# Performance work log

Measured on AMD Instinct MI355X. Metric: run time of the kernel, lower is better.

## Reference

```python
import jax, jax.numpy as jnp
import numpy as np

D_MODEL = 512
NUM_HEADS = 8
WINDOW = 64
HEAD_DIM = D_MODEL // NUM_HEADS


def setup_inputs() -> dict:
    key = jax.random.key(0)
    k1, k2, k3 = jax.random.split(key, 3)
    B, F, L, D = 4, 16, 2048, D_MODEL
    x = jax.random.normal(k1, (B, F, L, D), dtype=jnp.float32)
    w_qkv = jax.random.normal(k2, (D, 3 * D), dtype=jnp.float32) * (1.0 / np.sqrt(D))
    b_qkv = jnp.zeros((3 * D,), dtype=jnp.float32)
    w_proj = jax.random.normal(k3, (D, D), dtype=jnp.float32) * (1.0 / np.sqrt(D))
    b_proj = jnp.zeros((D,), dtype=jnp.float32)
    return {"x": x, "w_qkv": w_qkv, "b_qkv": b_qkv, "w_proj": w_proj, "b_proj": b_proj}


def reference(x, w_qkv, b_qkv, w_proj, b_proj):
    B, F, L, D = x.shape
    W = WINDOW
    H, hd = NUM_HEADS, HEAD_DIM
    nw = L // W  # L chosen divisible by window_size; pad path is identity here
    # partition into windows: (B, F, nw, W, D)
    xw = x.reshape(B, F, nw, W, D)
    # fused QKV projection
    qkv = jnp.einsum('bfnwd,de->bfnwe', xw, w_qkv) + b_qkv  # (B,F,nw,W,3D)
    qkv = qkv.reshape(B, F, nw, W, 3, H, hd)
    q = qkv[..., 0, :, :]  # (B,F,nw,W,H,hd)
    k = qkv[..., 1, :, :]
    v = qkv[..., 2, :, :]
    scale = 1.0 / np.sqrt(hd).astype(np.float32)
    # per-window attention: scores (B,F,nw,H,W,W)
    scores = jnp.einsum('bfnqhd,bfnkhd->bfnhqk', q, k) * scale
    attn = jax.nn.softmax(scores, axis=-1)
    out = jnp.einsum('bfnhqk,bfnkhd->bfnqhd', attn, v)  # (B,F,nw,W,H,hd)
    out = out.reshape(B, F, nw, W, D)
    out = jnp.einsum('bfnwd,de->bfnwe', out, w_proj) + b_proj
    return out.reshape(B, F, L, D)
```

## Files before the change

kernel.cpp:

```cpp
#include <hip/hip_runtime.h>

typedef __attribute__((ext_vector_type(8))) short short8;
typedef __attribute__((ext_vector_type(4))) float f32x4;
typedef unsigned short u16;
typedef unsigned int u32;

__device__ __forceinline__ u16 f2bf(float f){
  union { float f; u32 u; } v; v.f = f;
  u32 u = v.u;
  u32 r = (u + 0x7FFFu + ((u >> 16) & 1u)) >> 16;
  return (u16)r;
}

__device__ __forceinline__ u32 cvtpk(float a, float b){
  u32 r;
  asm("v_cvt_pk_bf16_f32 %0, %1, %2" : "=v"(r) : "v"(a), "v"(b));
  return r;
}

__device__ __forceinline__ int swz(int row, int cb){ return cb ^ ((row & 7) << 4); }

__device__ __forceinline__ void gload16(const void* g, void* l){
  __builtin_amdgcn_global_load_lds(
      (const __attribute__((address_space(1))) unsigned int*)g,
      (__attribute__((address_space(3))) unsigned int*)l, 16, 0, 0);
}

__global__ void convert_weights_frag(const float* __restrict__ wqkv,
                                     const float* __restrict__ wproj,
                                     u16* __restrict__ wqf,
                                     u16* __restrict__ wpf){
  int c = blockIdx.x * 256 + threadIdx.x;
  union { u16 u[8]; uint4 v; } t;
  if (c < 98304){
    int bn = c >> 13;
    int r  = c & 8191;
    int kt = r >> 10;
    int q  = r & 1023;
    int nsub = q >> 7;
    int ks = (q >> 6) & 1;
    int l  = q & 63;
    int e  = bn*128 + nsub*16 + (l & 15);
    int k0 = kt*64 + ks*32 + (l >> 4)*8;
    #pragma unroll
    for (int i = 0; i < 8; ++i) t.u[i] = f2bf(wqkv[(long)(k0 + i) * 1536 + e]);
    *reinterpret_cast<uint4*>(wqf + (long)c * 8) = t.v;
  } else {
    int c2 = c - 98304;
    int cb = c2 >> 12;
    int r  = c2 & 4095;
    int hh = r >> 9;
    int q  = r & 511;
    int n  = q >> 7;
    int ks = (q >> 6) & 1;
    int l  = q & 63;
    int e  = cb*64 + n*16 + (l & 15);
    int k0 = hh*64 + ks*32 + (l >> 4)*8;
    #pragma unroll
    for (int i = 0; i < 8; ++i) t.u[i] = f2bf(wproj[(long)(k0 + i) * 512 + e]);
    *reinterpret_cast<uint4*>(wpf + (long)c2 * 8) = t.v;
  }
}

__global__ void convert_x(const float* __restrict__ x, u16* __restrict__ xbf){
  int c = blockIdx.x * 256 + threadIdx.x;
  int tile = c >> 10, row = (c >> 3) & 127, c7 = c & 7;
  int bm = tile >> 3, kt = tile & 7;
  int j  = c7 ^ (row & 7);
  const float* src = x + (long)(bm * 128 + row) * 512 + kt * 64 + j * 8;
  float4 v0 = *reinterpret_cast<const float4*>(src);
  float4 v1 = *reinterpret_cast<const float4*>(src + 4);
  union { u16 u[8]; uint4 v; } t;
  t.u[0] = f2bf(v0.x); t.u[1] = f2bf(v0.y); t.u[2] = f2bf(v0.z); t.u[3] = f2bf(v0.w);
  t.u[4] = f2bf(v1.x); t.u[5] = f2bf(v1.y); t.u[6] = f2bf(v1.z); t.u[7] = f2bf(v1.w);
  *reinterpret_cast<uint4*>(xbf + (long)c * 8) = t.v;
}

__global__ __launch_bounds__(256, 3) void qkv_gemm128(
    const u16*  __restrict__ xbf,
    const u16*  __restrict__ wqf,
    const float* __restrict__ bqkv,
    u16* __restrict__ qkv)
{
  __shared__ char smem[34816];

  const int tid = threadIdx.x;
  const int l = tid & 63, w = tid >> 6;
  const int g = l >> 4,  ln = l & 15;
  const int wm = w >> 1, wn = w & 1;

  int hb   = blockIdx.x;
  int work = (hb & 7) * 1536 + (hb >> 3);
  int bn   = work % 12;
  int bm   = work / 12;

  f32x4 acc[4][4];
  #pragma unroll
  for (int m = 0; m < 4; ++m)
    #pragma unroll
    for (int n = 0; n < 4; ++n) acc[m][n] = (f32x4){0.f,0.f,0.f,0.f};

  const char* abase = (const char*)(xbf + (long)(bm * 8) * 8192);
  const u16*  bbase = wqf + (long)bn * 65536;

  auto stageA = [&](int kt, int slot){
    const char* src = abase + (long)kt * 16384;
    char* dst = smem + slot * 16384;
    #pragma unroll
    for (int i = 0; i < 4; ++i)
      gload16(src + (i*256 + tid)*16, dst + i*4096 + w*1024);
  };

  stageA(0, 0); stageA(1, 1);
  asm volatile("s_waitcnt vmcnt(4)" ::: "memory");
  __builtin_amdgcn_s_barrier();

  for (int t = 0; t < 8; ++t){
    short8 b[4][2];
    #pragma unroll
    for (int n = 0; n < 4; ++n)
      #pragma unroll
      for (int ks = 0; ks < 2; ++ks)
        b[n][ks] = *reinterpret_cast<const short8*>(
            bbase + ((((long)t*8 + wn*4 + n)*2 + ks)*64 + l)*8);
    const char* Ab = smem + (t & 1) * 16384;
    short8 a[4][2];
    #pragma unroll
    for (int m = 0; m < 4; ++m){
      int r = wm*64 + m*16 + ln;
      #pragma unroll
      for (int ks = 0; ks < 2; ++ks)
        a[m][ks] = *reinterpret_cast<const short8*>(
            Ab + r*128 + (((ks*4 + g) ^ (r & 7)) << 4));
    }
    asm volatile("s_waitcnt lgkmcnt(0)" ::: "memory");
    __builtin_amdgcn_s_barrier();
    if (t < 6) stageA(t + 2, t & 1);
    __builtin_amdgcn_s_setprio(1);
    #pragma unroll
    for (int m = 0; m < 4; ++m)
      #pragma unroll
      for (int n = 0; n < 4; ++n)
        #pragma unroll
        for (int ks = 0; ks < 2; ++ks)
          acc[m][n] = __builtin_amdgcn_mfma_f32_16x16x32_bf16(
              a[m][ks], b[n][ks], acc[m][n], 0, 0, 0);
    __builtin_amdgcn_s_setprio(0);
    if (t < 6)       asm volatile("s_waitcnt vmcnt(4)" ::: "memory");
    else if (t == 6) asm volatile("s_waitcnt vmcnt(0)" ::: "memory");
    if (t < 7) __builtin_amdgcn_s_barrier();
  }

  u16* ldsC = (u16*)smem;
  #pragma unroll
  for (int n = 0; n < 4; ++n){
    int col  = wn*64 + n*16 + ln;
    float bias = bqkv[bn*128 + col];
    #pragma unroll
    for (int m = 0; m < 4; ++m){
      int r0 = wm*64 + m*16 + g*4;
      #pragma unroll
      for (int r = 0; r < 4; ++r)
        ldsC[(r0 + r) * 136 + col] = f2bf(acc[m][n][r] + bias);
    }
  }
  __syncthreads();
  {
    int row = tid >> 1, half = tid & 1;
    const char* src = (const char*)(ldsC + row * 136 + half * 64);
    char* dst = (char*)qkv + ((long)(bm*128 + row) * 1536 + bn*128 + half*64) * 2;
    #pragma unroll
    for (int j = 0; j < 8; ++j)
      *reinterpret_cast<uint4*>(dst + j*16) = *reinterpret_cast<const uint4*>(src + j*16);
  }
}

__global__ __launch_bounds__(512, 4) void winattn_proj(
    const u16* __restrict__ qkv,
    const u16* __restrict__ wpf,
    const float* __restrict__ bproj,
    float* __restrict__ out)
{
  __shared__ u16 lds[8][4096];
  const int tid = threadIdx.x;
  const int l = tid & 63, w = tid >> 6;
  const int g = l >> 4,  ln = l & 15;
  const int gh = g >> 1, gl = g & 1;
  const long tokb = (long)blockIdx.x * 64;
  u16* vt = lds[w];
  const int h = w;

  {
    const int dg = l & 3, tg = l >> 2;
    uint4 vr[4][2];
    #pragma unroll
    for (int r = 0; r < 4; ++r){
      const char* vrow = (const char*)(qkv + (tokb + tg*4 + r) * 1536 + 1024 + h*64 + dg*16);
      vr[r][0] = *reinterpret_cast<const uint4*>(vrow);
      vr[r][1] = *reinterpret_cast<const uint4*>(vrow + 16);
    }
    #pragma unroll
    for (int dd = 0; dd < 16; ++dd){
      int d = dg*16 + dd;
      int sub = dd & 7, hi = dd >> 3;
      uint2 pk;
      pk.x = (u32)((const u16*)&vr[0][hi])[sub] | ((u32)((const u16*)&vr[1][hi])[sub] << 16);
      pk.y = (u32)((const u16*)&vr[2][hi])[sub] | ((u32)((const u16*)&vr[3][hi])[sub] << 16);
      *reinterpret_cast<uint2*>((char*)vt + d*128 + swz(d, tg*8)) = pk;
    }
  }

  f32x4 oacc[4][4];
  #pragma unroll
  for (int m = 0; m < 4; ++m)
    #pragma unroll
    for (int n = 0; n < 4; ++n) oacc[m][n] = (f32x4){0.f,0.f,0.f,0.f};

  const int lnA = ln + 32*gl;

  #pragma unroll
  for (int half = 0; half < 2; ++half){
    short8 qa[2][2];
    #pragma unroll
    for (int j = 0; j < 2; ++j){
      const char* qrow = (const char*)(qkv + (tokb + (half*2+j)*16 + ln) * 1536 + h*64 + g*8);
      qa[j][0] = *reinterpret_cast<const short8*>(qrow);
      qa[j][1] = *reinterpret_cast<const short8*>(qrow + 64);
    }
    f32x4 st[4][2];
    #pragma unroll
    for (int mk = 0; mk < 4; ++mk){
      st[mk][0] = (f32x4){0.f,0.f,0.f,0.f};
      st[mk][1] = (f32x4){0.f,0.f,0.f,0.f};
    }
    #pragma unroll
    for (int mk = 0; mk < 4; ++mk){
      const char* krow = (const char*)(qkv + (tokb + mk*16 + ln) * 1536 + 512 + h*64 + g*8);
      short8 kb0 = *reinterpret_cast<const short8*>(krow);
      short8 kb1 = *reinterpret_cast<const short8*>(krow + 64);
      #pragma unroll
      for (int j = 0; j < 2; ++j){
        st[mk][j] = __builtin_amdgcn_mfma_f32_16x16x32_bf16(kb0, qa[j][0], st[mk][j], 0, 0, 0);
        st[mk][j] = __builtin_amdgcn_mfma_f32_16x16x32_bf16(kb1, qa[j][1], st[mk][j], 0, 0, 0);
      }
    }
    u32 warr[4][2][2];
    #pragma unroll
    for (int j = 0; j < 2; ++j){
      float mx = -3.4e38f;
      #pragma unroll
      for (int mk = 0; mk < 4; ++mk)
        #pragma unroll
        for (int r = 0; r < 4; ++r) mx = fmaxf(mx, st[mk][j][r]);
      mx = fmaxf(mx, __shfl_xor(mx, 16, 64));
      mx = fmaxf(mx, __shfl_xor(mx, 32, 64));
      float s = 0.f;
      #pragma unroll
      for (int mk = 0; mk < 4; ++mk)
        #pragma unroll
        for (int r = 0; r < 4; ++r){
          float p = __expf((st[mk][j][r] - mx) * 0.125f);
          st[mk][j][r] = p; s += p;
        }
      s += __shfl_xor(s, 16, 64);
      s += __shfl_xor(s, 32, 64);
      float inv = 1.f / s;
      #pragma unroll
      for (int mk = 0; mk < 4; ++mk){
        warr[mk][j][0] = cvtpk(st[mk][j][0]*inv, st[mk][j][1]*inv);
        warr[mk][j][1] = cvtpk(st[mk][j][2]*inv, st[mk][j][3]*inv);
      }
    }
    __builtin_amdgcn_s_setprio(1);
    #pragma unroll
    for (int ks = 0; ks < 2; ++ks){
      short8 vb[4];
      #pragma unroll
      for (int n = 0; n < 4; ++n){
        int row = n*16 + ln;
        vb[n] = *reinterpret_cast<const short8*>((char*)vt + row*128 + swz(row, (ks*32 + g*8)*2));
      }
      #pragma unroll
      for (int mo = 0; mo < 2; ++mo){
        int m = half*2 + mo;
        u32 c0a = warr[2*ks  ][mo][0], c0b = warr[2*ks  ][mo][1];
        u32 c1a = warr[2*ks+1][mo][0], c1b = warr[2*ks+1][mo][1];
        u32 s0a = (u32)__shfl((int)c0a, lnA, 64);
        u32 s1a = (u32)__shfl((int)c1a, lnA, 64);
        u32 s0b = (u32)__shfl((int)c0b, lnA, 64);
        u32 s1b = (u32)__shfl((int)c1b, lnA, 64);
        u32 t0a = (u32)__shfl((int)c0a, lnA+16, 64);
        u32 t1a = (u32)__shfl((int)c1a, lnA+16, 64);
        u32 t0b = (u32)__shfl((int)c0b, lnA+16, 64);
        u32 t1b = (u32)__shfl((int)c1b, lnA+16, 64);
        union { u32 u[4]; short8 v; } pf;
        pf.u[0] = gh ? s1a : s0a;
        pf.u[1] = gh ? s1b : s0b;
        pf.u[2] = gh ? t1a : t0a;
        pf.u[3] = gh ? t1b : t0b;
        #pragma unroll
        for (int n = 0; n < 4; ++n)
          oacc[m][n] = __builtin_amdgcn_mfma_f32_16x16x32_bf16(pf.v, vb[n], oacc[m][n], 0, 0, 0);
      }
    }
    __builtin_amdgcn_s_setprio(0);
  }

  #pragma unroll
  for (int m = 0; m < 4; ++m)
    #pragma unroll
    for (int n = 0; n < 4; ++n){
      int d = n*16 + ln;
      #pragma unroll
      for (int r = 0; r < 4; ++r){
        int t = m*16 + g*4 + r;
        *reinterpret_cast<u16*>((char*)vt + t*128 + swz(t, d*2)) = f2bf(oacc[m][n][r]);
      }
    }

  __syncthreads();

  f32x4 acc[4][4];
  #pragma unroll
  for (int m = 0; m < 4; ++m)
    #pragma unroll
    for (int n = 0; n < 4; ++n) acc[m][n] = (f32x4){0.f,0.f,0.f,0.f};

  for (int hh = 0; hh < 8; ++hh){
    const char* obuf = (const char*)lds[hh];
    #pragma unroll
    for (int ks = 0; ks < 2; ++ks){
      short8 a[4], b[4];
      #pragma unroll
      for (int m = 0; m < 4; ++m){
        int row = m*16 + ln;
        a[m] = *reinterpret_cast<const short8*>(obuf + row*128 + swz(row, (ks*32 + g*8)*2));
      }
      #pragma unroll
      for (int n = 0; n < 4; ++n)
        b[n] = *reinterpret_cast<const short8*>(
            wpf + ((((long)w*8 + hh)*4 + n)*2 + ks)*512 + (long)l*8);
      __builtin_amdgcn_s_setprio(1);
      #pragma unroll
      for (int m = 0; m < 4; ++m)
        #pragma unroll
        for (int n = 0; n < 4; ++n)
          acc[m][n] = __builtin_amdgcn_mfma_f32_16x16x32_bf16(a[m], b[n], acc[m][n], 0, 0, 0);
      __builtin_amdgcn_s_setprio(0);
    }
  }

  #pragma unroll
  for (int n = 0; n < 4; ++n){
    int col = w*64 + n*16 + ln;
    float bias = bproj[col];
    #pragma unroll
    for (int m = 0; m < 4; ++m){
      #pragma unroll
      for (int r = 0; r < 4; ++r){
        int t = m*16 + g*4 + r;
        out[(tokb + t) * 512 + col] = acc[m][n][r] + bias;
      }
    }
  }
}

__global__ void convert_weights(const float* __restrict__ wqkv,
                                const float* __restrict__ wproj,
                                u16* __restrict__ wqkvt,
                                u16* __restrict__ wprojt){
  int tid = blockIdx.x * 256 + threadIdx.x;
  union { u16 u[8]; uint4 v; } tmp;
  if (tid < 1536 * 64){
    int e  = tid >> 6;
    int kc = (tid & 63) << 3;
    #pragma unroll
    for (int i = 0; i < 8; ++i) tmp.u[i] = f2bf(wqkv[(long)(kc + i) * 1536 + e]);
    *reinterpret_cast<uint4*>(wqkvt + (long)e * 512 + kc) = tmp.v;
  } else {
    int t2 = tid - 1536 * 64;
    int c  = t2 >> 6;
    int kc = (t2 & 63) << 3;
    #pragma unroll
    for (int i = 0; i < 8; ++i) tmp.u[i] = f2bf(wproj[(long)(kc + i) * 512 + c]);
    *reinterpret_cast<uint4*>(wprojt + (long)c * 512 + kc) = tmp.v;
  }
}

__global__ __launch_bounds__(512, 2) void fused_winattn(
    const float* __restrict__ x,
    const u16*  __restrict__ wqkvt,
    const float* __restrict__ bqkv,
    const u16*  __restrict__ wprojt,
    const float* __restrict__ bproj,
    float* __restrict__ out)
{
  __shared__ u16 lds_x[64 * 512];
  __shared__ u16 lds_q[64 * 64];
  __shared__ u16 lds_k[64 * 64];
  __shared__ u16 lds_vt[64 * 64];
  __shared__ u16 lds_p[64 * 64];

  const int tid = threadIdx.x;
  const int l   = tid & 63;
  const int w   = tid >> 6;
  const int g   = l >> 4;
  const int ln  = l & 15;
  const long tokbase = (long)blockIdx.x * 64;

  {
    const float4* xv = reinterpret_cast<const float4*>(x + tokbase * 512);
    #pragma unroll
    for (int j = 0; j < 16; ++j){
      int i   = j * 512 + tid;
      int row = i >> 7;
      int c4  = i & 127;
      float4 v = xv[i];
      uint2 pk;
      pk.x = (u32)f2bf(v.x) | ((u32)f2bf(v.y) << 16);
      pk.y = (u32)f2bf(v.z) | ((u32)f2bf(v.w) << 16);
      int byte = row * 1024 + swz(row, c4 * 8);
      *reinterpret_cast<uint2*>(reinterpret_cast<char*>(lds_x) + byte) = pk;
    }
  }

  f32x4 oacc[4][4];
  #pragma unroll
  for (int m = 0; m < 4; ++m)
    #pragma unroll
    for (int n = 0; n < 4; ++n) oacc[m][n] = (f32x4){0.f, 0.f, 0.f, 0.f};

  const int mw   = w & 3;
  const int half = w >> 2;

  __syncthreads();

  for (int h = 0; h < 8; ++h){
    f32x4 qacc[6];
    #pragma unroll
    for (int j = 0; j < 6; ++j) qacc[j] = (f32x4){0.f, 0.f, 0.f, 0.f};
    int ebase[6];
    #pragma unroll
    for (int j = 0; j < 6; ++j){
      int nt = half * 6 + j;
      int sec = nt >> 2;
      ebase[j] = sec * 512 + h * 64 + (nt & 3) * 16;
    }
    const int arow = mw * 16 + ln;
    #pragma unroll
    for (int ks = 0; ks < 16; ++ks){
      short8 a = *reinterpret_cast<const short8*>(
          reinterpret_cast<const char*>(lds_x) + arow * 1024 + swz(arow, (ks * 32 + g * 8) * 2));
      #pragma unroll
      for (int j = 0; j < 6; ++j){
        short8 b = *reinterpret_cast<const short8*>(
            wqkvt + (long)(ebase[j] + ln) * 512 + ks * 32 + g * 8);
        qacc[j] = __builtin_amdgcn_mfma_f32_16x16x32_bf16(a, b, qacc[j], 0, 0, 0);
      }
    }
    #pragma unroll
    for (int j = 0; j < 6; ++j){
      int nt  = half * 6 + j;
      int sec = nt >> 2;
      float bias = bqkv[ebase[j] + ln];
      if (sec < 2){
        u16* dst = (sec == 0) ? lds_q : lds_k;
        int c = (nt & 3) * 16 + ln;
        #pragma unroll
        for (int r = 0; r < 4; ++r){
          int t = mw * 16 + g * 4 + r;
          int byte = t * 128 + swz(t, c * 2);
          *reinterpret_cast<u16*>(reinterpret_cast<char*>(dst) + byte) = f2bf(qacc[j][r] + bias);
        }
      } else {
        int d  = (nt & 3) * 16 + ln;
        int t0 = mw * 16 + g * 4;
        uint2 pk;
        pk.x = (u32)f2bf(qacc[j][0] + bias) | ((u32)f2bf(qacc[j][1] + bias) << 16);
        pk.y = (u32)f2bf(qacc[j][2] + bias) | ((u32)f2bf(qacc[j][3] + bias) << 16);
        int byte = d * 128 + swz(d, t0 * 2);
        *reinterpret_cast<uint2*>(reinterpret_cast<char*>(lds_vt) + byte) = pk;
      }
    }
    __syncthreads();

    if (w < 4){
      f32x4 sacc[4];
      #pragma unroll
      for (int jt = 0; jt < 4; ++jt) sacc[jt] = (f32x4){0.f, 0.f, 0.f, 0.f};
      #pragma unroll
      for (int ks = 0; ks < 2; ++ks){
        int qrow = w * 16 + ln;
        short8 a = *reinterpret_cast<const short8*>(
            reinterpret_cast<const char*>(lds_q) + qrow * 128 + swz(qrow, (ks * 32 + g * 8) * 2));
        #pragma unroll
        for (int jt = 0; jt < 4; ++jt){
          int krow = jt * 16 + ln;
          short8 b = *reinterpret_cast<const short8*>(
              reinterpret_cast<const char*>(lds_k) + krow * 128 + swz(krow, (ks * 32 + g * 8) * 2));
          sacc[jt] = __builtin_amdgcn_mfma_f32_16x16x32_bf16(a, b, sacc[jt], 0, 0, 0);
        }
      }
      #pragma unroll
      for (int r = 0; r < 4; ++r){
        float mx = fmaxf(fmaxf(sacc[0][r], sacc[1][r]), fmaxf(sacc[2][r], sacc[3][r]));
        mx = fmaxf(mx, __shfl_xor(mx, 1, 64));
        mx = fmaxf(mx, __shfl_xor(mx, 2, 64));
        mx = fmaxf(mx, __shfl_xor(mx, 4, 64));
        mx = fmaxf(mx, __shfl_xor(mx, 8, 64));
        float p[4], s = 0.f;
        #pragma unroll
        for (int jt = 0; jt < 4; ++jt){
          p[jt] = __expf((sacc[jt][r] - mx) * 0.125f);
          s += p[jt];
        }
        s += __shfl_xor(s, 1, 64);
        s += __shfl_xor(s, 2, 64);
        s += __shfl_xor(s, 4, 64);
        s += __shfl_xor(s, 8, 64);
        float inv = 1.f / s;
        int i = w * 16 + g * 4 + r;
        #pragma unroll
        for (int jt = 0; jt < 4; ++jt){
          int c = jt * 16 + ln;
          int byte = i * 128 + swz(i, c * 2);
          *reinterpret_cast<u16*>(reinterpret_cast<char*>(lds_p) + byte) = f2bf(p[jt] * inv);
        }
      }
    }
    __syncthreads();

    {
      int mc  = w & 3;
      int nc0 = (w >> 2) * 2;
      f32x4 oc[2];
      oc[0] = (f32x4){0.f, 0.f, 0.f, 0.f};
      oc[1] = (f32x4){0.f, 0.f, 0.f, 0.f};
      #pragma unroll
      for (int ks = 0; ks < 2; ++ks){
        int prow = mc * 16 + ln;
        short8 a = *reinterpret_cast<const short8*>(
            reinterpret_cast<const char*>(lds_p) + prow * 128 + swz(prow, (ks * 32 + g * 8) * 2));
        #pragma unroll
        for (int jj = 0; jj < 2; ++jj){
          int vrow = (nc0 + jj) * 16 + ln;
          short8 b = *reinterpret_cast<const short8*>(
              reinterpret_cast<const char*>(lds_vt) + vrow * 128 + swz(vrow, (ks * 32 + g * 8) * 2));
          oc[jj] = __builtin_amdgcn_mfma_f32_16x16x32_bf16(a, b, oc[jj], 0, 0, 0);
        }
      }
      #pragma unroll
      for (int jj = 0; jj < 2; ++jj){
        int d = (nc0 + jj) * 16 + ln;
        #pragma unroll
        for (int r = 0; r < 4; ++r){
          int t = mc * 16 + g * 4 + r;
          int byte = t * 128 + swz(t, d * 2);
          *reinterpret_cast<u16*>(reinterpret_cast<char*>(lds_q) + byte) = f2bf(oc[jj][r]);
        }
      }
    }
    __syncthreads();

    #pragma unroll
    for (int ks = 0; ks < 2; ++ks){
      short8 a[4];
      #pragma unroll
      for (int m = 0; m < 4; ++m){
        int row = m * 16 + ln;
        a[m] = *reinterpret_cast<const short8*>(
            reinterpret_cast<const char*>(lds_q) + row * 128 + swz(row, (ks * 32 + g * 8) * 2));
      }
      #pragma unroll
      for (int nt = 0; nt < 4; ++nt){
        int e = w * 64 + nt * 16 + ln;
        short8 b = *reinterpret_cast<const short8*>(
            wprojt + (long)e * 512 + h * 64 + ks * 32 + g * 8);
        #pragma unroll
        for (int m = 0; m < 4; ++m)
          oacc[m][nt] = __builtin_amdgcn_mfma_f32_16x16x32_bf16(a[m], b, oacc[m][nt], 0, 0, 0);
      }
    }
    __syncthreads();
  }

  #pragma unroll
  for (int nt = 0; nt < 4; ++nt){
    int col = w * 64 + nt * 16 + ln;
    float bias = bproj[col];
    #pragma unroll
    for (int m = 0; m < 4; ++m){
      #pragma unroll
      for (int r = 0; r < 4; ++r){
        int t = m * 16 + g * 4 + r;
        out[(tokbase + t) * 512 + col] = oacc[m][nt][r] + bias;
      }
    }
  }
}

extern "C" void kernel_launch(void* const* d_in, const int* in_sizes, int n_in,
                              void* d_out, int out_size, void* d_ws, size_t ws_size,
                              hipStream_t stream) {
  const float* x     = (const float*)d_in[0];
  const float* wqkv  = (const float*)d_in[1];
  const float* bqkv  = (const float*)d_in[2];
  const float* wproj = (const float*)d_in[3];
  const float* bproj = (const float*)d_in[4];
  float* out = (float*)d_out;

  const size_t NEED = 538968064ULL;
  if (ws_size >= NEED){
    u16* wqf = (u16*)d_ws;
    u16* wpf = (u16*)((char*)d_ws + 1572864);
    u16* xbf = (u16*)((char*)d_ws + 2097152);
    u16* qkv = (u16*)((char*)d_ws + 136314880);
    convert_weights_frag<<<512, 256, 0, stream>>>(wqkv, wproj, wqf, wpf);
    convert_x<<<32768, 256, 0, stream>>>(x, xbf);
    qkv_gemm128<<<12288, 256, 0, stream>>>(xbf, wqf, bqkv, qkv);
    winattn_proj<<<2048, 512, 0, stream>>>(qkv, wpf, bproj, out);
  } else {
    u16* wqkvt  = (u16*)d_ws;
    u16* wprojt = wqkvt + 1536 * 512;
    convert_weights<<<512, 256, 0, stream>>>(wqkv, wproj, wqkvt, wprojt);
    fused_winattn<<<2048, 512, 0, stream>>>(x, wqkvt, bqkv, wprojt, bproj, out);
  }
}
```

Baseline: 582.6 us.

## Fuse x conversion, QKV GEMM, window attention and projection into one kernel

Replaces the separate x-to-bf16 conversion, QKV GEMM, and attention+projection kernels with a single kernel per 64-token window. The window's x rows are converted into LDS, and each wave (one head) computes its Q, K, V slices from weight fragments read directly from global memory, then runs attention and the output projection. This removes the large bf16 x and QKV intermediate round-trips through HBM and cuts the workspace requirement. In exchange it uses much more LDS per block (launch bounds drop to 2 blocks per CU) and loses the pipelined global-to-LDS staging of the old GEMM, so weight fragment loads may be less latency-hidden.

```diff
diff --git a/kernel.cpp b/kernel.cpp
--- a/kernel.cpp
+++ b/kernel.cpp
@@ -19,12 +19,6 @@
 }
 
 __device__ __forceinline__ int swz(int row, int cb){ return cb ^ ((row & 7) << 4); }
-
-__device__ __forceinline__ void gload16(const void* g, void* l){
-  __builtin_amdgcn_global_load_lds(
-      (const __attribute__((address_space(1))) unsigned int*)g,
-      (__attribute__((address_space(3))) unsigned int*)l, 16, 0, 0);
-}
 
 __global__ void convert_weights_frag(const float* __restrict__ wqkv,
                                      const float* __restrict__ wproj,
@@ -62,272 +56,236 @@
   }
 }
 
-__global__ void convert_x(const float* __restrict__ x, u16* __restrict__ xbf){
-  int c = blockIdx.x * 256 + threadIdx.x;
-  int tile = c >> 10, row = (c >> 3) & 127, c7 = c & 7;
-  int bm = tile >> 3, kt = tile & 7;
-  int j  = c7 ^ (row & 7);
-  const float* src = x + (long)(bm * 128 + row) * 512 + kt * 64 + j * 8;
-  float4 v0 = *reinterpret_cast<const float4*>(src);
-  float4 v1 = *reinterpret_cast<const float4*>(src + 4);
-  union { u16 u[8]; uint4 v; } t;
-  t.u[0] = f2bf(v0.x); t.u[1] = f2bf(v0.y); t.u[2] = f2bf(v0.z); t.u[3] = f2bf(v0.w);
-  t.u[4] = f2bf(v1.x); t.u[5] = f2bf(v1.y); t.u[6] = f2bf(v1.z); t.u[7] = f2bf(v1.w);
-  *reinterpret_cast<uint4*>(xbf + (long)c * 8) = t.v;
-}
-
-__global__ __launch_bounds__(256, 3) void qkv_gemm128(
-    const u16*  __restrict__ xbf,
+__global__ __launch_bounds__(512, 2) void fused_all(
+    const float* __restrict__ x,
     const u16*  __restrict__ wqf,
     const float* __restrict__ bqkv,
-    u16* __restrict__ qkv)
-{
-  __shared__ char smem[34816];
-
-  const int tid = threadIdx.x;
-  const int l = tid & 63, w = tid >> 6;
-  const int g = l >> 4,  ln = l & 15;
-  const int wm = w >> 1, wn = w & 1;
-
-  int hb   = blockIdx.x;
-  int work = (hb & 7) * 1536 + (hb >> 3);
-  int bn   = work % 12;
-  int bm   = work / 12;
-
-  f32x4 acc[4][4];
-  #pragma unroll
-  for (int m = 0; m < 4; ++m)
-    #pragma unroll
-    for (int n = 0; n < 4; ++n) acc[m][n] = (f32x4){0.f,0.f,0.f,0.f};
-
-  const char* abase = (const char*)(xbf + (long)(bm * 8) * 8192);
-  const u16*  bbase = wqf + (long)bn * 65536;
-
-  auto stageA = [&](int kt, int slot){
-    const char* src = abase + (long)kt * 16384;
-    char* dst = smem + slot * 16384;
-    #pragma unroll
-    for (int i = 0; i < 4; ++i)
-      gload16(src + (i*256 + tid)*16, dst + i*4096 + w*1024);
-  };
-
-  stageA(0, 0); stageA(1, 1);
-  asm volatile("s_waitcnt vmcnt(4)" ::: "memory");
-  __builtin_amdgcn_s_barrier();
-
-  for (int t = 0; t < 8; ++t){
-    short8 b[4][2];
-    #pragma unroll
-    for (int n = 0; n < 4; ++n)
-      #pragma unroll
-      for (int ks = 0; ks < 2; ++ks)
-        b[n][ks] = *reinterpret_cast<const short8*>(
-            bbase + ((((long)t*8 + wn*4 + n)*2 + ks)*64 + l)*8);
-    const char* Ab = smem + (t & 1) * 16384;
-    short8 a[4][2];
-    #pragma unroll
-    for (int m = 0; m < 4; ++m){
-      int r = wm*64 + m*16 + ln;
-      #pragma unroll
-      for (int ks = 0; ks < 2; ++ks)
-        a[m][ks] = *reinterpret_cast<const short8*>(
-            Ab + r*128 + (((ks*4 + g) ^ (r & 7)) << 4));
-    }
-    asm volatile("s_waitcnt lgkmcnt(0)" ::: "memory");
-    __builtin_amdgcn_s_barrier();
-    if (t < 6) stageA(t + 2, t & 1);
-    __builtin_amdgcn_s_setprio(1);
-    #pragma unroll
-    for (int m = 0; m < 4; ++m)
-      #pragma unroll
-      for (int n = 0; n < 4; ++n)
-        #pragma unroll
-        for (int ks = 0; ks < 2; ++ks)
-          acc[m][n] = __builtin_amdgcn_mfma_f32_16x16x32_bf16(
-              a[m][ks], b[n][ks], acc[m][n], 0, 0, 0);
-    __builtin_amdgcn_s_setprio(0);
-    if (t < 6)       asm volatile("s_waitcnt vmcnt(4)" ::: "memory");
-    else if (t == 6) asm volatile("s_waitcnt vmcnt(0)" ::: "memory");
-    if (t < 7) __builtin_amdgcn_s_barrier();
-  }
-
-  u16* ldsC = (u16*)smem;
-  #pragma unroll
-  for (int n = 0; n < 4; ++n){
-    int col  = wn*64 + n*16 + ln;
-    float bias = bqkv[bn*128 + col];
-    #pragma unroll
-    for (int m = 0; m < 4; ++m){
-      int r0 = wm*64 + m*16 + g*4;
-      #pragma unroll
-      for (int r = 0; r < 4; ++r)
-        ldsC[(r0 + r) * 136 + col] = f2bf(acc[m][n][r] + bias);
-    }
-  }
-  __syncthreads();
-  {
-    int row = tid >> 1, half = tid & 1;
-    const char* src = (const char*)(ldsC + row * 136 + half * 64);
-    char* dst = (char*)qkv + ((long)(bm*128 + row) * 1536 + bn*128 + half*64) * 2;
-    #pragma unroll
-    for (int j = 0; j < 8; ++j)
-      *reinterpret_cast<uint4*>(dst + j*16) = *reinterpret_cast<const uint4*>(src + j*16);
-  }
-}
-
-__global__ __launch_bounds__(512, 4) void winattn_proj(
-    const u16* __restrict__ qkv,
-    const u16* __restrict__ wpf,
+    const u16*  __restrict__ wpf,
     const float* __restrict__ bproj,
     float* __restrict__ out)
 {
-  __shared__ u16 lds[8][4096];
+  __shared__ u16 xw[64 * 512];
+  __shared__ u16 slots[8][4096];
+
   const int tid = threadIdx.x;
   const int l = tid & 63, w = tid >> 6;
   const int g = l >> 4,  ln = l & 15;
   const int gh = g >> 1, gl = g & 1;
   const long tokb = (long)blockIdx.x * 64;
-  u16* vt = lds[w];
   const int h = w;
+  u16* slot = slots[w];
 
   {
-    const int dg = l & 3, tg = l >> 2;
-    uint4 vr[4][2];
-    #pragma unroll
-    for (int r = 0; r < 4; ++r){
-      const char* vrow = (const char*)(qkv + (tokb + tg*4 + r) * 1536 + 1024 + h*64 + dg*16);
-      vr[r][0] = *reinterpret_cast<const uint4*>(vrow);
-      vr[r][1] = *reinterpret_cast<const uint4*>(vrow + 16);
-    }
-    #pragma unroll
-    for (int dd = 0; dd < 16; ++dd){
-      int d = dg*16 + dd;
-      int sub = dd & 7, hi = dd >> 3;
+    const float4* xv = reinterpret_cast<const float4*>(x + tokb * 512);
+    #pragma unroll
+    for (int i = 0; i < 16; ++i){
+      int idx = i * 512 + tid;
+      int row = idx >> 7, c4 = idx & 127;
+      float4 v = xv[idx];
       uint2 pk;
-      pk.x = (u32)((const u16*)&vr[0][hi])[sub] | ((u32)((const u16*)&vr[1][hi])[sub] << 16);
-      pk.y = (u32)((const u16*)&vr[2][hi])[sub] | ((u32)((const u16*)&vr[3][hi])[sub] << 16);
-      *reinterpret_cast<uint2*>((char*)vt + d*128 + swz(d, tg*8)) = pk;
-    }
-  }
-
-  f32x4 oacc[4][4];
-  #pragma unroll
-  for (int m = 0; m < 4; ++m)
-    #pragma unroll
-    for (int n = 0; n < 4; ++n) oacc[m][n] = (f32x4){0.f,0.f,0.f,0.f};
-
-  const int lnA = ln + 32*gl;
-
-  #pragma unroll
-  for (int half = 0; half < 2; ++half){
-    short8 qa[2][2];
-    #pragma unroll
-    for (int j = 0; j < 2; ++j){
-      const char* qrow = (const char*)(qkv + (tokb + (half*2+j)*16 + ln) * 1536 + h*64 + g*8);
-      qa[j][0] = *reinterpret_cast<const short8*>(qrow);
-      qa[j][1] = *reinterpret_cast<const short8*>(qrow + 64);
-    }
-    f32x4 st[4][2];
-    #pragma unroll
-    for (int mk = 0; mk < 4; ++mk){
-      st[mk][0] = (f32x4){0.f,0.f,0.f,0.f};
-      st[mk][1] = (f32x4){0.f,0.f,0.f,0.f};
-    }
-    #pragma unroll
-    for (int mk = 0; mk < 4; ++mk){
-      const char* krow = (const char*)(qkv + (tokb + mk*16 + ln) * 1536 + 512 + h*64 + g*8);
-      short8 kb0 = *reinterpret_cast<const short8*>(krow);
-      short8 kb1 = *reinterpret_cast<const short8*>(krow + 64);
-      #pragma unroll
-      for (int j = 0; j < 2; ++j){
-        st[mk][j] = __builtin_amdgcn_mfma_f32_16x16x32_bf16(kb0, qa[j][0], st[mk][j], 0, 0, 0);
-        st[mk][j] = __builtin_amdgcn_mfma_f32_16x16x32_bf16(kb1, qa[j][1], st[mk][j], 0, 0, 0);
-      }
-    }
-    u32 warr[4][2][2];
-    #pragma unroll
-    for (int j = 0; j < 2; ++j){
-      float mx = -3.4e38f;
-      #pragma unroll
-      for (int mk = 0; mk < 4; ++mk)
-        #pragma unroll
-        for (int r = 0; r < 4; ++r) mx = fmaxf(mx, st[mk][j][r]);
-      mx = fmaxf(mx, __shfl_xor(mx, 16, 64));
-      mx = fmaxf(mx, __shfl_xor(mx, 32, 64));
-      float s = 0.f;
-      #pragma unroll
-      for (int mk = 0; mk < 4; ++mk)
-        #pragma unroll
-        for (int r = 0; r < 4; ++r){
-          float p = __expf((st[mk][j][r] - mx) * 0.125f);
-          st[mk][j][r] = p; s += p;
-        }
-      s += __shfl_xor(s, 16, 64);
-      s += __shfl_xor(s, 32, 64);
-      float inv = 1.f / s;
-      #pragma unroll
-      for (int mk = 0; mk < 4; ++mk){
-        warr[mk][j][0] = cvtpk(st[mk][j][0]*inv, st[mk][j][1]*inv);
-        warr[mk][j][1] = cvtpk(st[mk][j][2]*inv, st[mk][j][3]*inv);
-      }
-    }
-    __builtin_amdgcn_s_setprio(1);
-    #pragma unroll
-    for (int ks = 0; ks < 2; ++ks){
-      short8 vb[4];
-      #pragma unroll
-      for (int n = 0; n < 4; ++n){
-        int row = n*16 + ln;
-        vb[n] = *reinterpret_cast<const short8*>((char*)vt + row*128 + swz(row, (ks*32 + g*8)*2));
-      }
-      #pragma unroll
-      for (int mo = 0; mo < 2; ++mo){
-        int m = half*2 + mo;
-        u32 c0a = warr[2*ks  ][mo][0], c0b = warr[2*ks  ][mo][1];
-        u32 c1a = warr[2*ks+1][mo][0], c1b = warr[2*ks+1][mo][1];
-        u32 s0a = (u32)__shfl((int)c0a, lnA, 64);
-        u32 s1a = (u32)__shfl((int)c1a, lnA, 64);
-        u32 s0b = (u32)__shfl((int)c0b, lnA, 64);
-        u32 s1b = (u32)__shfl((int)c1b, lnA, 64);
-        u32 t0a = (u32)__shfl((int)c0a, lnA+16, 64);
-        u32 t1a = (u32)__shfl((int)c1a, lnA+16, 64);
-        u32 t0b = (u32)__shfl((int)c0b, lnA+16, 64);
-        u32 t1b = (u32)__shfl((int)c1b, lnA+16, 64);
-        union { u32 u[4]; short8 v; } pf;
-        pf.u[0] = gh ? s1a : s0a;
-        pf.u[1] = gh ? s1b : s0b;
-        pf.u[2] = gh ? t1a : t0a;
-        pf.u[3] = gh ? t1b : t0b;
+      pk.x = cvtpk(v.x, v.y);
+      pk.y = cvtpk(v.z, v.w);
+      *reinterpret_cast<uint2*>(reinterpret_cast<char*>(xw) + row*1024 + swz(row, c4*8)) = pk;
+    }
+  }
+  __syncthreads();
+
+  f32x4 acc[4][4];
+  auto gemmQKV = [&](int s){
+    #pragma unroll
+    for (int m = 0; m < 4; ++m)
+      #pragma unroll
+      for (int n = 0; n < 4; ++n) acc[m][n] = (f32x4){0.f,0.f,0.f,0.f};
+    const u16* bb = wqf + (long)(s*4 + (h >> 1)) * 65536;
+    const int nsb = (h & 1) * 4;
+    #pragma unroll
+    for (int kk = 0; kk < 16; ++kk){
+      short8 bf[4], af[4];
+      #pragma unroll
+      for (int n = 0; n < 4; ++n)
+        bf[n] = *reinterpret_cast<const short8*>(
+            bb + ((((kk>>1)*8 + nsb + n)*2 + (kk & 1))*64 + l)*8);
+      #pragma unroll
+      for (int m = 0; m < 4; ++m){
+        int r = m*16 + ln;
+        af[m] = *reinterpret_cast<const short8*>(
+            reinterpret_cast<const char*>(xw) + r*1024 + swz(r, (kk*32 + g*8)*2));
+      }
+      __builtin_amdgcn_s_setprio(1);
+      #pragma unroll
+      for (int m = 0; m < 4; ++m)
         #pragma unroll
         for (int n = 0; n < 4; ++n)
-          oacc[m][n] = __builtin_amdgcn_mfma_f32_16x16x32_bf16(pf.v, vb[n], oacc[m][n], 0, 0, 0);
-      }
-    }
-    __builtin_amdgcn_s_setprio(0);
-  }
-
-  #pragma unroll
-  for (int m = 0; m < 4; ++m)
+          acc[m][n] = __builtin_amdgcn_mfma_f32_16x16x32_bf16(af[m], bf[n], acc[m][n], 0, 0, 0);
+      __builtin_amdgcn_s_setprio(0);
+    }
+  };
+
+  auto accToRows = [&](int boff){
     #pragma unroll
     for (int n = 0; n < 4; ++n){
       int d = n*16 + ln;
+      float bias = bqkv[boff + h*64 + d];
+      #pragma unroll
+      for (int m = 0; m < 4; ++m)
+        #pragma unroll
+        for (int r = 0; r < 4; ++r){
+          int t = m*16 + g*4 + r;
+          *reinterpret_cast<u16*>(reinterpret_cast<char*>(slot) + t*128 + swz(t, d*2)) =
+              f2bf(acc[m][n][r] + bias);
+        }
+    }
+  };
+
+  short8 qa[4][2], kb[4][2];
+
+  gemmQKV(0);
+  accToRows(0);
+  asm volatile("s_waitcnt lgkmcnt(0)" ::: "memory");
+  #pragma unroll
+  for (int j = 0; j < 4; ++j){
+    int r = j*16 + ln;
+    #pragma unroll
+    for (int ks = 0; ks < 2; ++ks)
+      qa[j][ks] = *reinterpret_cast<const short8*>(
+          reinterpret_cast<const char*>(slot) + r*128 + swz(r, (ks*32 + g*8)*2));
+  }
+  asm volatile("s_waitcnt lgkmcnt(0)" ::: "memory");
+
+  gemmQKV(1);
+  accToRows(512);
+  asm volatile("s_waitcnt lgkmcnt(0)" ::: "memory");
+  #pragma unroll
+  for (int mk = 0; mk < 4; ++mk){
+    int r = mk*16 + ln;
+    #pragma unroll
+    for (int ks = 0; ks < 2; ++ks)
+      kb[mk][ks] = *reinterpret_cast<const short8*>(
+          reinterpret_cast<const char*>(slot) + r*128 + swz(r, (ks*32 + g*8)*2));
+  }
+  asm volatile("s_waitcnt lgkmcnt(0)" ::: "memory");
+
+  gemmQKV(2);
+  #pragma unroll
+  for (int n = 0; n < 4; ++n){
+    int d = n*16 + ln;
+    float bias = bqkv[1024 + h*64 + d];
+    #pragma unroll
+    for (int m = 0; m < 4; ++m){
+      uint2 pk;
+      pk.x = cvtpk(acc[m][n][0] + bias, acc[m][n][1] + bias);
+      pk.y = cvtpk(acc[m][n][2] + bias, acc[m][n][3] + bias);
+      *reinterpret_cast<uint2*>(reinterpret_cast<char*>(slot) + d*128 + swz(d, (m*16 + g*4)*2)) = pk;
+    }
+  }
+  asm volatile("s_waitcnt lgkmcnt(0)" ::: "memory");
+
+  f32x4 st[4][4];
+  #pragma unroll
+  for (int mk = 0; mk < 4; ++mk)
+    #pragma unroll
+    for (int j = 0; j < 4; ++j) st[mk][j] = (f32x4){0.f,0.f,0.f,0.f};
+  __builtin_amdgcn_s_setprio(1);
+  #pragma unroll
+  for (int mk = 0; mk < 4; ++mk)
+    #pragma unroll
+    for (int j = 0; j < 4; ++j)
+      #pragma unroll
+      for (int ks = 0; ks < 2; ++ks)
+        st[mk][j] = __builtin_amdgcn_mfma_f32_16x16x32_bf16(kb[mk][ks], qa[j][ks], st[mk][j], 0, 0, 0);
+  __builtin_amdgcn_s_setprio(0);
+
+  u32 warr[4][4][2];
+  #pragma unroll
+  for (int j = 0; j < 4; ++j){
+    float mx = -3.4e38f;
+    #pragma unroll
+    for (int mk = 0; mk < 4; ++mk)
+      #pragma unroll
+      for (int r = 0; r < 4; ++r) mx = fmaxf(mx, st[mk][j][r]);
+    mx = fmaxf(mx, __shfl_xor(mx, 16, 64));
+    mx = fmaxf(mx, __shfl_xor(mx, 32, 64));
+    float s = 0.f;
+    #pragma unroll
+    for (int mk = 0; mk < 4; ++mk)
+      #pragma unroll
+      for (int r = 0; r < 4; ++r){
+        float p = __expf((st[mk][j][r] - mx) * 0.125f);
+        st[mk][j][r] = p; s += p;
+      }
+    s += __shfl_xor(s, 16, 64);
+    s += __shfl_xor(s, 32, 64);
+    float inv = 1.f / s;
+    #pragma unroll
+    for (int mk = 0; mk < 4; ++mk){
+      warr[mk][j][0] = cvtpk(st[mk][j][0]*inv, st[mk][j][1]*inv);
+      warr[mk][j][1] = cvtpk(st[mk][j][2]*inv, st[mk][j][3]*inv);
+    }
+  }
+
+  f32x4 oacc[4][4];
+  #pragma unroll
+  for (int m = 0; m < 4; ++m)
+    #pragma unroll
+    for (int n = 0; n < 4; ++n) oacc[m][n] = (f32x4){0.f,0.f,0.f,0.f};
+  const int lnA = ln + 32*gl;
+  #pragma unroll
+  for (int ks = 0; ks < 2; ++ks){
+    short8 vb[4];
+    #pragma unroll
+    for (int n = 0; n < 4; ++n){
+      int row = n*16 + ln;
+      vb[n] = *reinterpret_cast<const short8*>(
+          reinterpret_cast<const char*>(slot) + row*128 + swz(row, (ks*32 + g*8)*2));
+    }
+    __builtin_amdgcn_s_setprio(1);
+    #pragma unroll
+    for (int m = 0; m < 4; ++m){
+      u32 c0a = warr[2*ks  ][m][0], c0b = warr[2*ks  ][m][1];
+      u32 c1a = warr[2*ks+1][m][0], c1b = warr[2*ks+1][m][1];
+      u32 s0a = (u32)__shfl((int)c0a, lnA, 64);
+      u32 s1a = (u32)__shfl((int)c1a, lnA, 64);
+      u32 s0b = (u32)__shfl((int)c0b, lnA, 64);
+      u32 s1b = (u32)__shfl((int)c1b, lnA, 64);
+      u32 t0a = (u32)__shfl((int)c0a, lnA+16, 64);
+      u32 t1a = (u32)__shfl((int)c1a, lnA+16, 64);
+      u32 t0b = (u32)__shfl((int)c0b, lnA+16, 64);
+      u32 t1b = (u32)__shfl((int)c1b, lnA+16, 64);
+      union { u32 u[4]; short8 v; } pf;
+      pf.u[0] = gh ? s1a : s0a;
+      pf.u[1] = gh ? s1b : s0b;
+      pf.u[2] = gh ? t1a : t0a;
+      pf.u[3] = gh ? t1b : t0b;
+      #pragma unroll
+      for (int n = 0; n < 4; ++n)
+        oacc[m][n] = __builtin_amdgcn_mfma_f32_16x16x32_bf16(pf.v, vb[n], oacc[m][n], 0, 0, 0);
+    }
+    __builtin_amdgcn_s_setprio(0);
+  }
+
+  #pragma unroll
+  for (int m = 0; m < 4; ++m)
+    #pragma unroll
+    for (int n = 0; n < 4; ++n){
+      int d = n*16 + ln;
       #pragma unroll
       for (int r = 0; r < 4; ++r){
         int t = m*16 + g*4 + r;
-        *reinterpret_cast<u16*>((char*)vt + t*128 + swz(t, d*2)) = f2bf(oacc[m][n][r]);
+        *reinterpret_cast<u16*>(reinterpret_cast<char*>(slot) + t*128 + swz(t, d*2)) =
+            f2bf(oacc[m][n][r]);
       }
     }
 
   __syncthreads();
 
-  f32x4 acc[4][4];
+  f32x4 pacc[4][4];
   #pragma unroll
   for (int m = 0; m < 4; ++m)
     #pragma unroll
-    for (int n = 0; n < 4; ++n) acc[m][n] = (f32x4){0.f,0.f,0.f,0.f};
+    for (int n = 0; n < 4; ++n) pacc[m][n] = (f32x4){0.f,0.f,0.f,0.f};
 
   for (int hh = 0; hh < 8; ++hh){
-    const char* obuf = (const char*)lds[hh];
+    const char* obuf = (const char*)slots[hh];
     #pragma unroll
     for (int ks = 0; ks < 2; ++ks){
       short8 a[4], b[4];
@@ -345,7 +303,7 @@
       for (int m = 0; m < 4; ++m)
         #pragma unroll
         for (int n = 0; n < 4; ++n)
-          acc[m][n] = __builtin_amdgcn_mfma_f32_16x16x32_bf16(a[m], b[n], acc[m][n], 0, 0, 0);
+          pacc[m][n] = __builtin_amdgcn_mfma_f32_16x16x32_bf16(a[m], b[n], pacc[m][n], 0, 0, 0);
       __builtin_amdgcn_s_setprio(0);
     }
   }
@@ -359,7 +317,7 @@
       #pragma unroll
       for (int r = 0; r < 4; ++r){
         int t = m*16 + g*4 + r;
-        out[(tokb + t) * 512 + col] = acc[m][n][r] + bias;
+        out[(tokb + t) * 512 + col] = pacc[m][n][r] + bias;
       }
     }
   }
@@ -609,16 +567,12 @@
   const float* bproj = (const float*)d_in[4];
   float* out = (float*)d_out;
 
-  const size_t NEED = 538968064ULL;
+  const size_t NEED = 2097152ULL;
   if (ws_size >= NEED){
     u16* wqf = (u16*)d_ws;
     u16* wpf = (u16*)((char*)d_ws + 1572864);
-    u16* xbf = (u16*)((char*)d_ws + 2097152);
-    u16* qkv = (u16*)((char*)d_ws + 136314880);
     convert_weights_frag<<<512, 256, 0, stream>>>(wqkv, wproj, wqf, wpf);
-    convert_x<<<32768, 256, 0, stream>>>(x, xbf);
-    qkv_gemm128<<<12288, 256, 0, stream>>>(xbf, wqf, bqkv, qkv);
-    winattn_proj<<<2048, 512, 0, stream>>>(qkv, wpf, bproj, out);
+    fused_all<<<2048, 512, 0, stream>>>(x, wqf, bqkv, wpf, bproj, out);
   } else {
     u16* wqkvt  = (u16*)d_ws;
     u16* wprojt = wqkvt + 1536 * 512;
```

Result: slower. 643.1 us (+10.4%).

## Pre-fragment activations so QKV GEMM streams operands directly from global memory

Applied to the files above, without the earlier changes.

The bf16 conversion of x now writes activations in MFMA fragment order, mirroring the weight layout. The QKV GEMM then loads both A and B fragments directly from global memory into registers, dropping the LDS double-buffered staging, barriers and waitcnt choreography. LDS is now used only for the epilogue, and the occupancy hint rises to 4 blocks. The trade-off is that the two column-tile waves of a block each fetch the same A fragments from global/L2 with no shared LDS reuse, and there is no explicit prefetch overlap.

```diff
diff --git a/kernel.cpp b/kernel.cpp
--- a/kernel.cpp
+++ b/kernel.cpp
@@ -19,12 +19,6 @@
 }
 
 __device__ __forceinline__ int swz(int row, int cb){ return cb ^ ((row & 7) << 4); }
-
-__device__ __forceinline__ void gload16(const void* g, void* l){
-  __builtin_amdgcn_global_load_lds(
-      (const __attribute__((address_space(1))) unsigned int*)g,
-      (__attribute__((address_space(3))) unsigned int*)l, 16, 0, 0);
-}
 
 __global__ void convert_weights_frag(const float* __restrict__ wqkv,
                                      const float* __restrict__ wproj,
@@ -62,12 +56,16 @@
   }
 }
 
-__global__ void convert_x(const float* __restrict__ x, u16* __restrict__ xbf){
+__global__ void convert_x_frag(const float* __restrict__ x, u16* __restrict__ xbf){
   int c = blockIdx.x * 256 + threadIdx.x;
-  int tile = c >> 10, row = (c >> 3) & 127, c7 = c & 7;
-  int bm = tile >> 3, kt = tile & 7;
-  int j  = c7 ^ (row & 7);
-  const float* src = x + (long)(bm * 128 + row) * 512 + kt * 64 + j * 8;
+  int l    = c & 63;
+  int ks   = (c >> 6) & 1;
+  int msub = (c >> 7) & 7;
+  int kt   = (c >> 10) & 7;
+  int bm   = c >> 13;
+  int row  = bm*128 + msub*16 + (l & 15);
+  int k0   = kt*64 + ks*32 + (l >> 4)*8;
+  const float* src = x + (long)row * 512 + k0;
   float4 v0 = *reinterpret_cast<const float4*>(src);
   float4 v1 = *reinterpret_cast<const float4*>(src + 4);
   union { u16 u[8]; uint4 v; } t;
@@ -76,13 +74,13 @@
   *reinterpret_cast<uint4*>(xbf + (long)c * 8) = t.v;
 }
 
-__global__ __launch_bounds__(256, 3) void qkv_gemm128(
+__global__ __launch_bounds__(256, 4) void qkv_stream(
     const u16*  __restrict__ xbf,
     const u16*  __restrict__ wqf,
     const float* __restrict__ bqkv,
     u16* __restrict__ qkv)
 {
-  __shared__ char smem[34816];
+  __shared__ u16 ldsC[128 * 136];
 
   const int tid = threadIdx.x;
   const int l = tid & 63, w = tid >> 6;
@@ -100,42 +98,21 @@
     #pragma unroll
     for (int n = 0; n < 4; ++n) acc[m][n] = (f32x4){0.f,0.f,0.f,0.f};
 
-  const char* abase = (const char*)(xbf + (long)(bm * 8) * 8192);
-  const u16*  bbase = wqf + (long)bn * 65536;
-
-  auto stageA = [&](int kt, int slot){
-    const char* src = abase + (long)kt * 16384;
-    char* dst = smem + slot * 16384;
-    #pragma unroll
-    for (int i = 0; i < 4; ++i)
-      gload16(src + (i*256 + tid)*16, dst + i*4096 + w*1024);
-  };
-
-  stageA(0, 0); stageA(1, 1);
-  asm volatile("s_waitcnt vmcnt(4)" ::: "memory");
-  __builtin_amdgcn_s_barrier();
+  const u16* ap = xbf + (long)bm * 65536 + (((long)(wm*4)*2)*64 + l) * 8;
+  const u16* bp = wqf + (long)bn * 65536 + (((long)(wn*4)*2)*64 + l) * 8;
 
   for (int t = 0; t < 8; ++t){
-    short8 b[4][2];
+    short8 a[4][2], b[4][2];
+    #pragma unroll
+    for (int m = 0; m < 4; ++m)
+      #pragma unroll
+      for (int ks = 0; ks < 2; ++ks)
+        a[m][ks] = *reinterpret_cast<const short8*>(ap + ((m*2 + ks)*64)*8);
     #pragma unroll
     for (int n = 0; n < 4; ++n)
       #pragma unroll
       for (int ks = 0; ks < 2; ++ks)
-        b[n][ks] = *reinterpret_cast<const short8*>(
-            bbase + ((((long)t*8 + wn*4 + n)*2 + ks)*64 + l)*8);
-    const char* Ab = smem + (t & 1) * 16384;
-    short8 a[4][2];
-    #pragma unroll
-    for (int m = 0; m < 4; ++m){
-      int r = wm*64 + m*16 + ln;
-      #pragma unroll
-      for (int ks = 0; ks < 2; ++ks)
-        a[m][ks] = *reinterpret_cast<const short8*>(
-            Ab + r*128 + (((ks*4 + g) ^ (r & 7)) << 4));
-    }
-    asm volatile("s_waitcnt lgkmcnt(0)" ::: "memory");
-    __builtin_amdgcn_s_barrier();
-    if (t < 6) stageA(t + 2, t & 1);
+        b[n][ks] = *reinterpret_cast<const short8*>(bp + ((n*2 + ks)*64)*8);
     __builtin_amdgcn_s_setprio(1);
     #pragma unroll
     for (int m = 0; m < 4; ++m)
@@ -146,12 +123,10 @@
           acc[m][n] = __builtin_amdgcn_mfma_f32_16x16x32_bf16(
               a[m][ks], b[n][ks], acc[m][n], 0, 0, 0);
     __builtin_amdgcn_s_setprio(0);
-    if (t < 6)       asm volatile("s_waitcnt vmcnt(4)" ::: "memory");
-    else if (t == 6) asm volatile("s_waitcnt vmcnt(0)" ::: "memory");
-    if (t < 7) __builtin_amdgcn_s_barrier();
-  }
-
-  u16* ldsC = (u16*)smem;
+    ap += 8192;
+    bp += 8192;
+  }
+
   #pragma unroll
   for (int n = 0; n < 4; ++n){
     int col  = wn*64 + n*16 + ln;
@@ -616,8 +591,8 @@
     u16* xbf = (u16*)((char*)d_ws + 2097152);
     u16* qkv = (u16*)((char*)d_ws + 136314880);
     convert_weights_frag<<<512, 256, 0, stream>>>(wqkv, wproj, wqf, wpf);
-    convert_x<<<32768, 256, 0, stream>>>(x, xbf);
-    qkv_gemm128<<<12288, 256, 0, stream>>>(xbf, wqf, bqkv, qkv);
+    convert_x_frag<<<32768, 256, 0, stream>>>(x, xbf);
+    qkv_stream<<<12288, 256, 0, stream>>>(xbf, wqf, bqkv, qkv);
     winattn_proj<<<2048, 512, 0, stream>>>(qkv, wpf, bproj, out);
   } else {
     u16* wqkvt  = (u16*)d_ws;
```

Measured after the change: 807.7 us. +38.6%, slower.

## Fuse fp32-to-bf16 conversion of x into the QKV GEMM loader

Applied to the files above, without the earlier changes.

Removes the separate convert_x kernel and its bf16 workspace. The QKV GEMM now loads fp32 x tiles into registers, converts them with packed bf16 conversion, and writes them swizzled into double-buffered LDS. Register prefetch replaces the direct global-to-LDS loads. This cuts a full write and reread of the activation tensor, but each column block now reads twice as many bytes of x, and the register staging changes latency hiding.

```diff
diff --git a/kernel.cpp b/kernel.cpp
--- a/kernel.cpp
+++ b/kernel.cpp
@@ -19,12 +19,6 @@
 }
 
 __device__ __forceinline__ int swz(int row, int cb){ return cb ^ ((row & 7) << 4); }
-
-__device__ __forceinline__ void gload16(const void* g, void* l){
-  __builtin_amdgcn_global_load_lds(
-      (const __attribute__((address_space(1))) unsigned int*)g,
-      (__attribute__((address_space(3))) unsigned int*)l, 16, 0, 0);
-}
 
 __global__ void convert_weights_frag(const float* __restrict__ wqkv,
                                      const float* __restrict__ wproj,
@@ -62,22 +56,8 @@
   }
 }
 
-__global__ void convert_x(const float* __restrict__ x, u16* __restrict__ xbf){
-  int c = blockIdx.x * 256 + threadIdx.x;
-  int tile = c >> 10, row = (c >> 3) & 127, c7 = c & 7;
-  int bm = tile >> 3, kt = tile & 7;
-  int j  = c7 ^ (row & 7);
-  const float* src = x + (long)(bm * 128 + row) * 512 + kt * 64 + j * 8;
-  float4 v0 = *reinterpret_cast<const float4*>(src);
-  float4 v1 = *reinterpret_cast<const float4*>(src + 4);
-  union { u16 u[8]; uint4 v; } t;
-  t.u[0] = f2bf(v0.x); t.u[1] = f2bf(v0.y); t.u[2] = f2bf(v0.z); t.u[3] = f2bf(v0.w);
-  t.u[4] = f2bf(v1.x); t.u[5] = f2bf(v1.y); t.u[6] = f2bf(v1.z); t.u[7] = f2bf(v1.w);
-  *reinterpret_cast<uint4*>(xbf + (long)c * 8) = t.v;
-}
-
-__global__ __launch_bounds__(256, 3) void qkv_gemm128(
-    const u16*  __restrict__ xbf,
+__global__ __launch_bounds__(256, 3) void qkv_fused(
+    const float* __restrict__ x,
     const u16*  __restrict__ wqf,
     const float* __restrict__ bqkv,
     u16* __restrict__ qkv)
@@ -100,42 +80,56 @@
     #pragma unroll
     for (int n = 0; n < 4; ++n) acc[m][n] = (f32x4){0.f,0.f,0.f,0.f};
 
-  const char* abase = (const char*)(xbf + (long)(bm * 8) * 8192);
+  const int srow = tid & 127, shalf = tid >> 7;
+  const float* xsrc = x + (long)(bm*128 + srow) * 512 + shalf * 32;
   const u16*  bbase = wqf + (long)bn * 65536;
 
-  auto stageA = [&](int kt, int slot){
-    const char* src = abase + (long)kt * 16384;
-    char* dst = smem + slot * 16384;
-    #pragma unroll
-    for (int i = 0; i < 4; ++i)
-      gload16(src + (i*256 + tid)*16, dst + i*4096 + w*1024);
+  float4 xr[8];
+  auto gloadX = [&](int kt){
+    const float4* s = reinterpret_cast<const float4*>(xsrc + kt * 64);
+    #pragma unroll
+    for (int j = 0; j < 8; ++j) xr[j] = s[j];
   };
-
-  stageA(0, 0); stageA(1, 1);
-  asm volatile("s_waitcnt vmcnt(4)" ::: "memory");
+  auto writeX = [&](int slot){
+    char* dst = smem + slot*16384 + srow*128;
+    #pragma unroll
+    for (int jj = 0; jj < 4; ++jj){
+      uint4 v;
+      v.x = cvtpk(xr[jj*2].x,   xr[jj*2].y);
+      v.y = cvtpk(xr[jj*2].z,   xr[jj*2].w);
+      v.z = cvtpk(xr[jj*2+1].x, xr[jj*2+1].y);
+      v.w = cvtpk(xr[jj*2+1].z, xr[jj*2+1].w);
+      *reinterpret_cast<uint4*>(dst + (((shalf*4 + jj) ^ (srow & 7)) << 4)) = v;
+    }
+  };
+
+  gloadX(0);
+  writeX(0);
+  asm volatile("s_waitcnt lgkmcnt(0)" ::: "memory");
+  gloadX(1);
   __builtin_amdgcn_s_barrier();
-
+  __builtin_amdgcn_sched_barrier(0);
+
+  short8 af[4][2], bf[4][2];
   for (int t = 0; t < 8; ++t){
-    short8 b[4][2];
+    if (t < 7) writeX((t + 1) & 1);
     #pragma unroll
     for (int n = 0; n < 4; ++n)
       #pragma unroll
       for (int ks = 0; ks < 2; ++ks)
-        b[n][ks] = *reinterpret_cast<const short8*>(
+        bf[n][ks] = *reinterpret_cast<const short8*>(
             bbase + ((((long)t*8 + wn*4 + n)*2 + ks)*64 + l)*8);
     const char* Ab = smem + (t & 1) * 16384;
-    short8 a[4][2];
     #pragma unroll
     for (int m = 0; m < 4; ++m){
       int r = wm*64 + m*16 + ln;
       #pragma unroll
       for (int ks = 0; ks < 2; ++ks)
-        a[m][ks] = *reinterpret_cast<const short8*>(
+        af[m][ks] = *reinterpret_cast<const short8*>(
             Ab + r*128 + (((ks*4 + g) ^ (r & 7)) << 4));
     }
     asm volatile("s_waitcnt lgkmcnt(0)" ::: "memory");
-    __builtin_amdgcn_s_barrier();
-    if (t < 6) stageA(t + 2, t & 1);
+    if (t < 6) gloadX(t + 2);
     __builtin_amdgcn_s_setprio(1);
     #pragma unroll
     for (int m = 0; m < 4; ++m)
@@ -144,13 +138,13 @@
         #pragma unroll
         for (int ks = 0; ks < 2; ++ks)
           acc[m][n] = __builtin_amdgcn_mfma_f32_16x16x32_bf16(
-              a[m][ks], b[n][ks], acc[m][n], 0, 0, 0);
+              af[m][ks], bf[n][ks], acc[m][n], 0, 0, 0);
     __builtin_amdgcn_s_setprio(0);
-    if (t < 6)       asm volatile("s_waitcnt vmcnt(4)" ::: "memory");
-    else if (t == 6) asm volatile("s_waitcnt vmcnt(0)" ::: "memory");
-    if (t < 7) __builtin_amdgcn_s_barrier();
-  }
-
+    __builtin_amdgcn_s_barrier();
+    __builtin_amdgcn_sched_barrier(0);
+  }
+
+  __syncthreads();
   u16* ldsC = (u16*)smem;
   #pragma unroll
   for (int n = 0; n < 4; ++n){
@@ -609,15 +603,13 @@
   const float* bproj = (const float*)d_in[4];
   float* out = (float*)d_out;
 
-  const size_t NEED = 538968064ULL;
+  const size_t NEED = 404750336ULL;
   if (ws_size >= NEED){
     u16* wqf = (u16*)d_ws;
     u16* wpf = (u16*)((char*)d_ws + 1572864);
-    u16* xbf = (u16*)((char*)d_ws + 2097152);
-    u16* qkv = (u16*)((char*)d_ws + 136314880);
+    u16* qkv = (u16*)((char*)d_ws + 2097152);
     convert_weights_frag<<<512, 256, 0, stream>>>(wqkv, wproj, wqf, wpf);
-    convert_x<<<32768, 256, 0, stream>>>(x, xbf);
-    qkv_gemm128<<<12288, 256, 0, stream>>>(xbf, wqf, bqkv, qkv);
+    qkv_fused<<<12288, 256, 0, stream>>>(x, wqf, bqkv, qkv);
     winattn_proj<<<2048, 512, 0, stream>>>(qkv, wpf, bproj, out);
   } else {
     u16* wqkvt  = (u16*)d_ws;
```

Result: slower. 800.6 us (+37.4%).
